# Kernel tuning notes

Measured on AMD Instinct MI355X. Metric: run time of the kernel, lower is better.

Reference implementation:

```python
import jax, jax.numpy as jnp
import numpy as np

N_ITEMS = 512
N_SAMPLES = 32768
WINDOW = 512
CHUNK = WINDOW // 2 + 1          # 257 rfft bins
N_COEFFS = CHUNK * 3             # 771: [mags | phases | start mags]
STEP = WINDOW // 2               # 256 hop
N_FRAMES = N_SAMPLES // STEP     # 128
BASE_RES = 0.5
SPAN = 1.0 - BASE_RES
EPS = 1e-12

_HANN = jnp.asarray(np.hanning(WINDOW), dtype=jnp.float32)


def setup_inputs() -> dict:
    key = jax.random.key(0)
    k1, k2, k3 = jax.random.split(key, 3)
    selections = jax.random.normal(k1, (8, 16, 4, N_ITEMS), dtype=jnp.float32)
    # init(x): uniform(-6, 6) * bernoulli(p=0.01)  -> sparse large-magnitude coeffs
    vals = jax.random.uniform(k2, (N_ITEMS, N_COEFFS), minval=-6.0, maxval=6.0, dtype=jnp.float32)
    mask = (jax.random.uniform(k3, (N_ITEMS, N_COEFFS)) < 0.01).astype(jnp.float32)
    items = vals * mask
    return {"selections": selections, "items": items}


def _resonance_synth(coeffs):
    # coeffs: (B, E, X, N_COEFFS)
    mags = BASE_RES + jax.nn.sigmoid(coeffs[..., :CHUNK]) * 0.9999 * SPAN       # decay per frame, in (0.5, 1)
    phases = jnp.tanh(coeffs[..., CHUNK:2 * CHUNK]) * jnp.pi                    # per-frame phase advance
    starts = jax.nn.sigmoid(coeffs[..., 2 * CHUNK:])                            # initial bin magnitudes

    # log-space cumulative decay scan across frames: mag at frame t = mags ** (t+1)
    t = jnp.arange(1, N_FRAMES + 1, dtype=jnp.float32)                          # (F,)
    log_m = jnp.log(mags + EPS)                                                 # (B,E,X,C)
    decay = jnp.exp(log_m[..., None, :] * t[:, None])                           # (B,E,X,F,C)
    phi = phases[..., None, :] * t[:, None]                                     # cumulative phase rotation

    spec = (starts[..., None, :] * decay).astype(jnp.complex64) * jnp.exp(1j * phi.astype(jnp.complex64))
    frames = jnp.fft.irfft(spec, n=WINDOW, axis=-1).astype(jnp.float32)         # (B,E,X,F,W)
    frames = frames * _HANN

    first = frames[..., :STEP]                                                  # (B,E,X,F,STEP)
    second = frames[..., STEP:]
    shifted = jnp.concatenate([jnp.zeros_like(second[..., :1, :]), second[..., :-1, :]], axis=-2)
    out = first + shifted                                                       # (B,E,X,F,STEP)
    return out.reshape(*frames.shape[:-2], N_FRAMES * STEP)                     # (B,E,X,N_SAMPLES)


def reference(selections, items):
    # select_items with selection_type='relu': non-negative mixture over the item table
    selected = jnp.einsum('bexi,ic->bexc', jax.nn.relu(selections), items)      # (B,E,X,N_COEFFS)
    res = _resonance_synth(selected)                                            # (B,E,X,N_SAMPLES)
    norm = jnp.linalg.norm(res, axis=-1, keepdims=True)
    return res / (norm + 1e-8)                                                  # unit_norm along samples
```

## Files before the change

### kernel.cpp

```cpp
#include <hip/hip_runtime.h>
#include <math.h>

#define N_ROWS   512
#define NBINS    257
#define N_COEFFS 771
#define STEP     256
#define N_FRAMES 128
#define N_SAMP   32768
#define KDIM     576
#define NCHUNK   18
#define PCH      9
#define PCOLS    288
#define TWO_PI   6.283185307179586f
#define CSC_CAP  64

typedef _Float16 half8 __attribute__((ext_vector_type(8)));
typedef float floatx4 __attribute__((ext_vector_type(4)));

__global__ __launch_bounds__(256) void k_csc(const float* __restrict__ items,
                                             int* __restrict__ cnt,
                                             int* __restrict__ idx,
                                             float* __restrict__ val) {
    int col  = blockIdx.x * 4 + (threadIdx.x >> 6);
    int lane = threadIdx.x & 63;
    if (col >= N_COEFFS) return;
    int base = 0;
    for (int i0 = 0; i0 < 512; i0 += 64) {
        float v = items[(size_t)(i0 + lane) * N_COEFFS + col];
        unsigned long long m = __ballot(v != 0.f);
        int pos = base + __popcll(m & ((1ull << lane) - 1ull));
        if (v != 0.f && pos < CSC_CAP) {
            idx[col * CSC_CAP + pos] = i0 + lane;
            val[col * CSC_CAP + pos] = v;
        }
        base += __popcll(m);
    }
    if (lane == 0) cnt[col] = base < CSC_CAP ? base : CSC_CAP;
}

__global__ __launch_bounds__(256) void k_prep(const float* __restrict__ sel,
                                              const int* __restrict__ csc_cnt,
                                              const int* __restrict__ csc_idx,
                                              const float* __restrict__ csc_val,
                                              float4* __restrict__ pa,
                                              float2* __restrict__ pb,
                                              _Float16* __restrict__ Bt) {
    int bid = blockIdx.x;
    int tid = threadIdx.x;
    if (bid < N_ROWS) {
        int row = bid;
        __shared__ float s[512];
        float v0 = sel[row * 512 + tid];
        float v1 = sel[row * 512 + tid + 256];
        s[tid]       = v0 > 0.f ? v0 : 0.f;
        s[tid + 256] = v1 > 0.f ? v1 : 0.f;
        __syncthreads();
        for (int k = tid; k < NBINS; k += 256) {
            float acc[3];
            #pragma unroll
            for (int ch = 0; ch < 3; ++ch) {
                int c = ch * NBINS + k;
                int n = csc_cnt[c];
                const int*   ip = csc_idx + c * CSC_CAP;
                const float* vp = csc_val + c * CSC_CAP;
                float a = 0.f;
                for (int j = 0; j < n; ++j)
                    a = fmaf(s[ip[j]], vp[j], a);
                acc[ch] = a;
            }
            float cm = acc[0], cp = acc[1], cs = acc[2];
            float sig_m = 1.f / (1.f + expf(-cm));
            float mag   = 0.5f + sig_m * 0.9999f * 0.5f;
            float lm    = logf(mag + 1e-12f);
            float ph    = tanhf(cp) * 3.14159265358979323846f;
            float sph, cph;
            sincosf(ph, &sph, &cph);
            float st = 1.f / (1.f + expf(-cs));
            float w  = (k == 0 || k == 256) ? (1.f / 512.f) : (2.f / 512.f);
            int indx = row * NBINS + k;
            pa[indx] = make_float4(lm, ph, cph, sph);
            pb[indx] = make_float2(st * w, mag);
        }
    } else {
        int jg = bid - N_ROWS;
        int n  = ((jg >> 7) << 6) + (jg & 63) + (((jg >> 6) & 1) << 8);
        for (int k = tid; k < KDIM; k += 256) {
            float v = 0.f;
            if (k < NBINS) {
                int r = (k * n) & 511;
                v = cosf(TWO_PI * (float)r * (1.f / 512.f));
            } else if (k < 2 * NBINS) {
                int r = ((k - NBINS) * n) & 511;
                v = -sinf(TWO_PI * (float)r * (1.f / 512.f));
            }
            size_t pos = ((size_t)((k >> 5) * 4 + ((k >> 3) & 3)) * 512 + jg) * 8 + (k & 7);
            Bt[pos] = (_Float16)v;
        }
    }
}

__global__ __launch_bounds__(512, 2) void k_row(const float4* __restrict__ pa,
                                                const float2* __restrict__ pb,
                                                const _Float16* __restrict__ basis,
                                                float* __restrict__ out) {
    __shared__ _Float16 Asm[PCH * 4096];
    __shared__ _Float16 Bsm[2][16384];
    __shared__ float    SBB[4][64];
    __shared__ float    red[8];

    const int row  = blockIdx.x;
    const int t    = threadIdx.x;
    const int lane = t & 63;
    const int w    = t >> 6;
    const int wm   = w >> 2;
    const int wn   = w & 3;
    const int quad = lane >> 4;
    const int l16  = lane & 15;

    auto agen = [&](int ph) {
        if (t < PCOLS) {
            int gc = ph * PCOLS + t;
            int bin; bool isCos;
            if (gc < NBINS)          { bin = gc;          isCos = true;  }
            else if (gc < 2 * NBINS) { bin = gc - NBINS;  isCos = false; }
            else                     { bin = 0;           isCos = true;  }
            float4 P = pa[row * NBINS + bin];
            float2 Q = pb[row * NBINS + bin];
            float D = 512.f * Q.x * Q.y;
            if (gc >= 2 * NBINS) D = 0.f;
            float c = P.z, s = P.w;
            int ch = t >> 5, g = (t >> 3) & 3, o = t & 7;
            _Float16* base = &Asm[ch * 4096 + o];
            for (int f = 0; f < N_FRAMES; ++f) {
                float val = isCos ? D * c : D * s;
                base[f * 32 + ((g ^ ((f >> 1) & 3) ^ ((f >> 3) & 3)) << 3)] = (_Float16)val;
                D *= Q.y;
                float nc = fmaf(c, P.z, -s * P.w);
                float ns = fmaf(s, P.z,  c * P.w);
                c = nc; s = ns;
            }
        }
    };

    half8 L[4];
    #pragma unroll
    for (int g = 0; g < 4; ++g)
        L[g] = *(const half8*)(basis + ((size_t)(0 * 4 + g) * 512 + t) * 8);
    agen(0);
    #pragma unroll
    for (int g = 0; g < 4; ++g)
        *(half8*)&Bsm[0][g * 4096 + t * 8] = L[g];
    #pragma unroll
    for (int g = 0; g < 4; ++g)
        L[g] = *(const half8*)(basis + ((size_t)(1 * 4 + g) * 512 + t) * 8);
    __syncthreads();

    floatx4 acc[4][8] = {};
    int p = 0;
    for (int ph = 0; ph < 2; ++ph) {
        if (ph == 1) { agen(1); __syncthreads(); }
        for (int ks = 0; ks < PCH; ++ks) {
            int gc = ph * PCH + ks;
            if (gc < NCHUNK - 1) {
                #pragma unroll
                for (int g = 0; g < 4; ++g)
                    *(half8*)&Bsm[p ^ 1][g * 4096 + t * 8] = L[g];
                if (gc < NCHUNK - 2) {
                    #pragma unroll
                    for (int g = 0; g < 4; ++g)
                        L[g] = *(const half8*)(basis + ((size_t)((gc + 2) * 4 + g) * 512 + t) * 8);
                }
            }
            half8 av[4];
            #pragma unroll
            for (int mt = 0; mt < 4; ++mt) {
                int m = wm * 64 + mt * 16 + l16;
                av[mt] = *(const half8*)&Asm[ks * 4096 + m * 32 +
                          ((quad ^ ((m >> 1) & 3) ^ ((m >> 3) & 3)) << 3)];
            }
            #pragma unroll
            for (int nt = 0; nt < 8; ++nt) {
                int u = wn * 128 + nt * 16 + l16;
                half8 bv = *(const half8*)&Bsm[p][quad * 4096 + u * 8];
                #pragma unroll
                for (int mt = 0; mt < 4; ++mt)
                    acc[mt][nt] = __builtin_amdgcn_mfma_f32_16x16x32_f16(av[mt], bv, acc[mt][nt], 0, 0, 0);
            }
            __syncthreads();
            p ^= 1;
        }
    }

    float h1[4], h2[4];
    #pragma unroll
    for (int nt = 0; nt < 4; ++nt) {
        int n1 = wn * 64 + nt * 16 + l16;
        h1[nt] = 0.5f - 0.5f * cosf(TWO_PI * (float)n1 / 511.f);
        h2[nt] = 0.5f - 0.5f * cosf(TWO_PI * (float)(n1 + 256) / 511.f);
    }
    if (wm == 0 && quad == 3) {
        #pragma unroll
        for (int nt = 0; nt < 4; ++nt)
            SBB[wn][nt * 16 + l16] = acc[3][nt + 4][3] * h2[nt];
    }
    __syncthreads();

    float oreg[4][4][4];
    float prevLast[4] = {0.f, 0.f, 0.f, 0.f};
    float ssq = 0.f;
    #pragma unroll
    for (int mt = 0; mt < 4; ++mt) {
        #pragma unroll
        for (int nt = 0; nt < 4; ++nt) {
            float W2[4];
            #pragma unroll
            for (int rr = 0; rr < 4; ++rr) W2[rr] = acc[mt][nt + 4][rr] * h2[nt];
            float tmp = (quad == 3) ? prevLast[nt] : W2[3];
            float carry = __shfl(tmp, (lane + 48) & 63, 64);
            if (mt == 0 && quad == 0)
                carry = (wm == 1) ? SBB[wn][nt * 16 + l16] : 0.f;
            float v = fmaf(acc[mt][nt][0], h1[nt], carry);
            oreg[mt][nt][0] = v; ssq = fmaf(v, v, ssq);
            #pragma unroll
            for (int rr = 1; rr < 4; ++rr) {
                v = fmaf(acc[mt][nt][rr], h1[nt], W2[rr - 1]);
                oreg[mt][nt][rr] = v; ssq = fmaf(v, v, ssq);
            }
            prevLast[nt] = W2[3];
        }
    }

    #pragma unroll
    for (int off = 32; off > 0; off >>= 1) ssq += __shfl_down(ssq, off, 64);
    if (lane == 0) red[w] = ssq;
    __syncthreads();
    float tot = red[0] + red[1] + red[2] + red[3] + red[4] + red[5] + red[6] + red[7];
    float scale = 1.f / (sqrtf(tot) + 1e-8f);

    float* orow = out + (size_t)row * N_SAMP;
    #pragma unroll
    for (int mt = 0; mt < 4; ++mt) {
        #pragma unroll
        for (int nt = 0; nt < 4; ++nt) {
            int n1 = wn * 64 + nt * 16 + l16;
            #pragma unroll
            for (int rr = 0; rr < 4; ++rr) {
                int f = wm * 64 + mt * 16 + quad * 4 + rr;
                orow[f * 256 + n1] = oreg[mt][nt][rr] * scale;
            }
        }
    }
}

extern "C" void kernel_launch(void* const* d_in, const int* in_sizes, int n_in,
                              void* d_out, int out_size, void* d_ws, size_t ws_size,
                              hipStream_t stream) {
    const float* sel   = (const float*)d_in[0];
    const float* items = (const float*)d_in[1];
    float* out = (float*)d_out;

    char* ws = (char*)d_ws;
    size_t off = 0;
    float4* pa   = (float4*)(ws + off); off += (size_t)N_ROWS * NBINS * 16;   off = (off + 255) & ~255ull;
    float2* pb   = (float2*)(ws + off); off += (size_t)N_ROWS * NBINS * 8;    off = (off + 255) & ~255ull;
    _Float16* basis = (_Float16*)(ws + off); off += (size_t)NCHUNK * 4 * 512 * 8 * 2; off = (off + 255) & ~255ull;
    int*   csc_cnt = (int*)(ws + off);   off += (size_t)N_COEFFS * 4;          off = (off + 255) & ~255ull;
    int*   csc_idx = (int*)(ws + off);   off += (size_t)N_COEFFS * CSC_CAP * 4; off = (off + 255) & ~255ull;
    float* csc_val = (float*)(ws + off); off += (size_t)N_COEFFS * CSC_CAP * 4;

    k_csc<<<dim3((N_COEFFS + 3) / 4), dim3(256), 0, stream>>>(items, csc_cnt, csc_idx, csc_val);
    k_prep<<<dim3(N_ROWS + 512), dim3(256), 0, stream>>>(sel, csc_cnt, csc_idx, csc_val, pa, pb, basis);
    k_row<<<dim3(N_ROWS), dim3(512), 0, stream>>>(pa, pb, basis, out);
}
```

Baseline: 154.3 us.

## Read DFT basis directly from global memory and generate both A phases upfront

The row kernel no longer stages basis (B) tiles in shared memory through a register double buffer. Each wave now loads its B fragments straight from global memory (cached in L2) inside the MFMA loop. Both halves of the A panel are generated into two shared buffers before the MFMA loops, so the per-chunk barriers go away and only one barrier remains between the halves. In exchange, the MFMA loop is now exposed to global load latency with no explicit prefetch, and shared memory use grows. The sparse-column builder also switches from one wave per column with ballot compaction to one thread per column scanning rows serially.

```diff
diff --git a/kernel.cpp b/kernel.cpp
--- a/kernel.cpp
+++ b/kernel.cpp
@@ -21,21 +21,18 @@
                                              int* __restrict__ cnt,
                                              int* __restrict__ idx,
                                              float* __restrict__ val) {
-    int col  = blockIdx.x * 4 + (threadIdx.x >> 6);
-    int lane = threadIdx.x & 63;
+    int col = blockIdx.x * 256 + threadIdx.x;
     if (col >= N_COEFFS) return;
-    int base = 0;
-    for (int i0 = 0; i0 < 512; i0 += 64) {
-        float v = items[(size_t)(i0 + lane) * N_COEFFS + col];
-        unsigned long long m = __ballot(v != 0.f);
-        int pos = base + __popcll(m & ((1ull << lane) - 1ull));
-        if (v != 0.f && pos < CSC_CAP) {
-            idx[col * CSC_CAP + pos] = i0 + lane;
-            val[col * CSC_CAP + pos] = v;
-        }
-        base += __popcll(m);
-    }
-    if (lane == 0) cnt[col] = base < CSC_CAP ? base : CSC_CAP;
+    int n = 0;
+    for (int i = 0; i < 512; ++i) {
+        float v = items[(size_t)i * N_COEFFS + col];
+        if (v != 0.f && n < CSC_CAP) {
+            idx[col * CSC_CAP + n] = i;
+            val[col * CSC_CAP + n] = v;
+            ++n;
+        }
+    }
+    cnt[col] = n;
 }
 
 __global__ __launch_bounds__(256) void k_prep(const float* __restrict__ sel,
@@ -103,8 +100,7 @@
                                                 const float2* __restrict__ pb,
                                                 const _Float16* __restrict__ basis,
                                                 float* __restrict__ out) {
-    __shared__ _Float16 Asm[PCH * 4096];
-    __shared__ _Float16 Bsm[2][16384];
+    __shared__ _Float16 Asm[2][PCH * 4096];
     __shared__ float    SBB[4][64];
     __shared__ float    red[8];
 
@@ -130,7 +126,7 @@
             if (gc >= 2 * NBINS) D = 0.f;
             float c = P.z, s = P.w;
             int ch = t >> 5, g = (t >> 3) & 3, o = t & 7;
-            _Float16* base = &Asm[ch * 4096 + o];
+            _Float16* base = &Asm[ph][ch * 4096 + o];
             for (int f = 0; f < N_FRAMES; ++f) {
                 float val = isCos ? D * c : D * s;
                 base[f * 32 + ((g ^ ((f >> 1) & 3) ^ ((f >> 3) & 3)) << 3)] = (_Float16)val;
@@ -142,52 +138,48 @@
         }
     };
 
-    half8 L[4];
-    #pragma unroll
-    for (int g = 0; g < 4; ++g)
-        L[g] = *(const half8*)(basis + ((size_t)(0 * 4 + g) * 512 + t) * 8);
+    const _Float16* bbase = basis + ((size_t)quad * 512 + wn * 128 + l16) * 8;
+
     agen(0);
-    #pragma unroll
-    for (int g = 0; g < 4; ++g)
-        *(half8*)&Bsm[0][g * 4096 + t * 8] = L[g];
-    #pragma unroll
-    for (int g = 0; g < 4; ++g)
-        L[g] = *(const half8*)(basis + ((size_t)(1 * 4 + g) * 512 + t) * 8);
     __syncthreads();
 
     floatx4 acc[4][8] = {};
-    int p = 0;
-    for (int ph = 0; ph < 2; ++ph) {
-        if (ph == 1) { agen(1); __syncthreads(); }
-        for (int ks = 0; ks < PCH; ++ks) {
-            int gc = ph * PCH + ks;
-            if (gc < NCHUNK - 1) {
-                #pragma unroll
-                for (int g = 0; g < 4; ++g)
-                    *(half8*)&Bsm[p ^ 1][g * 4096 + t * 8] = L[g];
-                if (gc < NCHUNK - 2) {
-                    #pragma unroll
-                    for (int g = 0; g < 4; ++g)
-                        L[g] = *(const half8*)(basis + ((size_t)((gc + 2) * 4 + g) * 512 + t) * 8);
-                }
-            }
-            half8 av[4];
-            #pragma unroll
-            for (int mt = 0; mt < 4; ++mt) {
-                int m = wm * 64 + mt * 16 + l16;
-                av[mt] = *(const half8*)&Asm[ks * 4096 + m * 32 +
-                          ((quad ^ ((m >> 1) & 3) ^ ((m >> 3) & 3)) << 3)];
-            }
-            #pragma unroll
-            for (int nt = 0; nt < 8; ++nt) {
-                int u = wn * 128 + nt * 16 + l16;
-                half8 bv = *(const half8*)&Bsm[p][quad * 4096 + u * 8];
-                #pragma unroll
-                for (int mt = 0; mt < 4; ++mt)
-                    acc[mt][nt] = __builtin_amdgcn_mfma_f32_16x16x32_f16(av[mt], bv, acc[mt][nt], 0, 0, 0);
-            }
-            __syncthreads();
-            p ^= 1;
+
+    agen(1);
+    for (int ks = 0; ks < PCH; ++ks) {
+        half8 av[4];
+        #pragma unroll
+        for (int mt = 0; mt < 4; ++mt) {
+            int m = wm * 64 + mt * 16 + l16;
+            av[mt] = *(const half8*)&Asm[0][ks * 4096 + m * 32 +
+                      ((quad ^ ((m >> 1) & 3) ^ ((m >> 3) & 3)) << 3)];
+        }
+        const _Float16* bc = bbase + (size_t)ks * 16384;
+        #pragma unroll
+        for (int nt = 0; nt < 8; ++nt) {
+            half8 bv = *(const half8*)(bc + nt * 128);
+            #pragma unroll
+            for (int mt = 0; mt < 4; ++mt)
+                acc[mt][nt] = __builtin_amdgcn_mfma_f32_16x16x32_f16(av[mt], bv, acc[mt][nt], 0, 0, 0);
+        }
+    }
+    __syncthreads();
+
+    for (int ks = 0; ks < PCH; ++ks) {
+        half8 av[4];
+        #pragma unroll
+        for (int mt = 0; mt < 4; ++mt) {
+            int m = wm * 64 + mt * 16 + l16;
+            av[mt] = *(const half8*)&Asm[1][ks * 4096 + m * 32 +
+                      ((quad ^ ((m >> 1) & 3) ^ ((m >> 3) & 3)) << 3)];
+        }
+        const _Float16* bc = bbase + (size_t)(PCH + ks) * 16384;
+        #pragma unroll
+        for (int nt = 0; nt < 8; ++nt) {
+            half8 bv = *(const half8*)(bc + nt * 128);
+            #pragma unroll
+            for (int mt = 0; mt < 4; ++mt)
+                acc[mt][nt] = __builtin_amdgcn_mfma_f32_16x16x32_f16(av[mt], bv, acc[mt][nt], 0, 0, 0);
         }
     }
 
@@ -268,7 +260,7 @@
     int*   csc_idx = (int*)(ws + off);   off += (size_t)N_COEFFS * CSC_CAP * 4; off = (off + 255) & ~255ull;
     float* csc_val = (float*)(ws + off); off += (size_t)N_COEFFS * CSC_CAP * 4;
 
-    k_csc<<<dim3((N_COEFFS + 3) / 4), dim3(256), 0, stream>>>(items, csc_cnt, csc_idx, csc_val);
+    k_csc<<<dim3((N_COEFFS + 255) / 256), dim3(256), 0, stream>>>(items, csc_cnt, csc_idx, csc_val);
     k_prep<<<dim3(N_ROWS + 512), dim3(256), 0, stream>>>(sel, csc_cnt, csc_idx, csc_val, pa, pb, basis);
     k_row<<<dim3(N_ROWS), dim3(512), 0, stream>>>(pa, pb, basis, out);
 }
```

Result: slower. 303.3 us (+96.5%).

## Build padded CSC via tiled transpose and merge basis generation into the CSC kernel

Applied to the files above, without the earlier changes.

The sparse column extraction now loads 64x64 tiles of the item table through shared memory, which gives coalesced reads instead of the strided per-column access. Each column is stored as a fixed set of 32 zero-padded entries, so the per-row mixing loop unrolls fully with no count array or data-dependent trip count. Basis generation moves into the same launch as the CSC build, and the parameter pass becomes its own kernel. The risk is that a column with more than 32 nonzeros would be silently truncated. The padded entries also add a few wasted FMAs per coefficient.

```diff
diff --git a/kernel.cpp b/kernel.cpp
--- a/kernel.cpp
+++ b/kernel.cpp
@@ -12,77 +12,20 @@
 #define PCH      9
 #define PCOLS    288
 #define TWO_PI   6.283185307179586f
-#define CSC_CAP  64
+#define PADN     32
+#define CSC_BLKS 13
 
 typedef _Float16 half8 __attribute__((ext_vector_type(8)));
 typedef float floatx4 __attribute__((ext_vector_type(4)));
 
-__global__ __launch_bounds__(256) void k_csc(const float* __restrict__ items,
-                                             int* __restrict__ cnt,
+__global__ __launch_bounds__(256) void k_pre(const float* __restrict__ items,
                                              int* __restrict__ idx,
-                                             float* __restrict__ val) {
-    int col  = blockIdx.x * 4 + (threadIdx.x >> 6);
-    int lane = threadIdx.x & 63;
-    if (col >= N_COEFFS) return;
-    int base = 0;
-    for (int i0 = 0; i0 < 512; i0 += 64) {
-        float v = items[(size_t)(i0 + lane) * N_COEFFS + col];
-        unsigned long long m = __ballot(v != 0.f);
-        int pos = base + __popcll(m & ((1ull << lane) - 1ull));
-        if (v != 0.f && pos < CSC_CAP) {
-            idx[col * CSC_CAP + pos] = i0 + lane;
-            val[col * CSC_CAP + pos] = v;
-        }
-        base += __popcll(m);
-    }
-    if (lane == 0) cnt[col] = base < CSC_CAP ? base : CSC_CAP;
-}
-
-__global__ __launch_bounds__(256) void k_prep(const float* __restrict__ sel,
-                                              const int* __restrict__ csc_cnt,
-                                              const int* __restrict__ csc_idx,
-                                              const float* __restrict__ csc_val,
-                                              float4* __restrict__ pa,
-                                              float2* __restrict__ pb,
-                                              _Float16* __restrict__ Bt) {
-    int bid = blockIdx.x;
-    int tid = threadIdx.x;
-    if (bid < N_ROWS) {
-        int row = bid;
-        __shared__ float s[512];
-        float v0 = sel[row * 512 + tid];
-        float v1 = sel[row * 512 + tid + 256];
-        s[tid]       = v0 > 0.f ? v0 : 0.f;
-        s[tid + 256] = v1 > 0.f ? v1 : 0.f;
-        __syncthreads();
-        for (int k = tid; k < NBINS; k += 256) {
-            float acc[3];
-            #pragma unroll
-            for (int ch = 0; ch < 3; ++ch) {
-                int c = ch * NBINS + k;
-                int n = csc_cnt[c];
-                const int*   ip = csc_idx + c * CSC_CAP;
-                const float* vp = csc_val + c * CSC_CAP;
-                float a = 0.f;
-                for (int j = 0; j < n; ++j)
-                    a = fmaf(s[ip[j]], vp[j], a);
-                acc[ch] = a;
-            }
-            float cm = acc[0], cp = acc[1], cs = acc[2];
-            float sig_m = 1.f / (1.f + expf(-cm));
-            float mag   = 0.5f + sig_m * 0.9999f * 0.5f;
-            float lm    = logf(mag + 1e-12f);
-            float ph    = tanhf(cp) * 3.14159265358979323846f;
-            float sph, cph;
-            sincosf(ph, &sph, &cph);
-            float st = 1.f / (1.f + expf(-cs));
-            float w  = (k == 0 || k == 256) ? (1.f / 512.f) : (2.f / 512.f);
-            int indx = row * NBINS + k;
-            pa[indx] = make_float4(lm, ph, cph, sph);
-            pb[indx] = make_float2(st * w, mag);
-        }
-    } else {
-        int jg = bid - N_ROWS;
+                                             float* __restrict__ val,
+                                             _Float16* __restrict__ Bt) {
+    const int bid = blockIdx.x;
+    const int tid = threadIdx.x;
+    if (bid >= CSC_BLKS) {
+        int jg = bid - CSC_BLKS;
         int n  = ((jg >> 7) << 6) + (jg & 63) + (((jg >> 6) & 1) << 8);
         for (int k = tid; k < KDIM; k += 256) {
             float v = 0.f;
@@ -96,6 +39,91 @@
             size_t pos = ((size_t)((k >> 5) * 4 + ((k >> 3) & 3)) * 512 + jg) * 8 + (k & 7);
             Bt[pos] = (_Float16)v;
         }
+        return;
+    }
+    __shared__ float tile[64][65];
+    __shared__ int   basec[64];
+    const int c0   = bid * 64;
+    const int w    = tid >> 6;
+    const int lane = tid & 63;
+    const int c    = c0 + lane;
+    if (tid < 64) basec[tid] = 0;
+    for (int r0 = 0; r0 < 512; r0 += 64) {
+        float v[16];
+        #pragma unroll
+        for (int rr = 0; rr < 16; ++rr)
+            v[rr] = (c < N_COEFFS) ? items[(size_t)(r0 + rr * 4 + w) * N_COEFFS + c] : 0.f;
+        #pragma unroll
+        for (int rr = 0; rr < 16; ++rr)
+            tile[rr * 4 + w][lane] = v[rr];
+        __syncthreads();
+        #pragma unroll
+        for (int cc = 0; cc < 16; ++cc) {
+            int cl   = w * 16 + cc;
+            int gcol = c0 + cl;
+            float x  = tile[lane][cl];
+            unsigned long long m = __ballot(x != 0.f);
+            int base = basec[cl];
+            int pos  = base + __popcll(m & ((1ull << lane) - 1ull));
+            if (gcol < N_COEFFS && x != 0.f && pos < PADN) {
+                idx[gcol * PADN + pos] = r0 + lane;
+                val[gcol * PADN + pos] = x;
+            }
+            if (lane == 0) basec[cl] = base + __popcll(m);
+        }
+        __syncthreads();
+    }
+    for (int j = tid; j < 64 * PADN; j += 256) {
+        int cl = j >> 5, pz = j & (PADN - 1);
+        int gcol = c0 + cl;
+        if (gcol < N_COEFFS) {
+            int b = basec[cl]; b = b < PADN ? b : PADN;
+            if (pz >= b) {
+                idx[gcol * PADN + pz] = 0;
+                val[gcol * PADN + pz] = 0.f;
+            }
+        }
+    }
+}
+
+__global__ __launch_bounds__(256) void k_params(const float* __restrict__ sel,
+                                                const int* __restrict__ csc_idx,
+                                                const float* __restrict__ csc_val,
+                                                float4* __restrict__ pa,
+                                                float2* __restrict__ pb) {
+    int row = blockIdx.x;
+    int tid = threadIdx.x;
+    __shared__ float s[512];
+    float v0 = sel[row * 512 + tid];
+    float v1 = sel[row * 512 + tid + 256];
+    s[tid]       = v0 > 0.f ? v0 : 0.f;
+    s[tid + 256] = v1 > 0.f ? v1 : 0.f;
+    __syncthreads();
+    for (int k = tid; k < NBINS; k += 256) {
+        float acc[3];
+        #pragma unroll
+        for (int ch = 0; ch < 3; ++ch) {
+            int cc = ch * NBINS + k;
+            const int*   ip = csc_idx + cc * PADN;
+            const float* vp = csc_val + cc * PADN;
+            float a = 0.f;
+            #pragma unroll
+            for (int j = 0; j < PADN; ++j)
+                a = fmaf(s[ip[j]], vp[j], a);
+            acc[ch] = a;
+        }
+        float cm = acc[0], cp = acc[1], cs = acc[2];
+        float sig_m = 1.f / (1.f + expf(-cm));
+        float mag   = 0.5f + sig_m * 0.9999f * 0.5f;
+        float lm    = logf(mag + 1e-12f);
+        float ph    = tanhf(cp) * 3.14159265358979323846f;
+        float sph, cph;
+        sincosf(ph, &sph, &cph);
+        float st = 1.f / (1.f + expf(-cs));
+        float w  = (k == 0 || k == 256) ? (1.f / 512.f) : (2.f / 512.f);
+        int indx = row * NBINS + k;
+        pa[indx] = make_float4(lm, ph, cph, sph);
+        pb[indx] = make_float2(st * w, mag);
     }
 }
 
@@ -264,11 +292,10 @@
     float4* pa   = (float4*)(ws + off); off += (size_t)N_ROWS * NBINS * 16;   off = (off + 255) & ~255ull;
     float2* pb   = (float2*)(ws + off); off += (size_t)N_ROWS * NBINS * 8;    off = (off + 255) & ~255ull;
     _Float16* basis = (_Float16*)(ws + off); off += (size_t)NCHUNK * 4 * 512 * 8 * 2; off = (off + 255) & ~255ull;
-    int*   csc_cnt = (int*)(ws + off);   off += (size_t)N_COEFFS * 4;          off = (off + 255) & ~255ull;
-    int*   csc_idx = (int*)(ws + off);   off += (size_t)N_COEFFS * CSC_CAP * 4; off = (off + 255) & ~255ull;
-    float* csc_val = (float*)(ws + off); off += (size_t)N_COEFFS * CSC_CAP * 4;
-
-    k_csc<<<dim3((N_COEFFS + 3) / 4), dim3(256), 0, stream>>>(items, csc_cnt, csc_idx, csc_val);
-    k_prep<<<dim3(N_ROWS + 512), dim3(256), 0, stream>>>(sel, csc_cnt, csc_idx, csc_val, pa, pb, basis);
+    int*   csc_idx = (int*)(ws + off);   off += (size_t)N_COEFFS * PADN * 4;  off = (off + 255) & ~255ull;
+    float* csc_val = (float*)(ws + off); off += (size_t)N_COEFFS * PADN * 4;
+
+    k_pre<<<dim3(CSC_BLKS + 512), dim3(256), 0, stream>>>(items, csc_idx, csc_val, basis);
+    k_params<<<dim3(N_ROWS), dim3(256), 0, stream>>>(sel, csc_idx, csc_val, pa, pb);
     k_row<<<dim3(N_ROWS), dim3(512), 0, stream>>>(pa, pb, basis, out);
 }
```

Result: slower. 171.8 us (+11.3%).
